# Kernel tuning notes

Hardware: AMD Instinct MI355X
Metric: run time of the kernel (lower is better)

The kernel has to match this reference:

```python
import jax, jax.numpy as jnp
import numpy as np

EPS = 1e-5

def _layernorm(x, g, b):
    mu = jnp.mean(x, axis=-1, keepdims=True)
    var = jnp.mean(jnp.square(x - mu), axis=-1, keepdims=True)
    return (x - mu) * jax.lax.rsqrt(var + EPS) * g + b

def setup_inputs() -> dict:
    key = jax.random.key(0)
    ks = jax.random.split(key, 5)
    T, B, C, E, V = 196, 64, 1024, 512, 32000
    return {
        "feat": jax.random.normal(ks[0], (T, B, C), dtype=jnp.float32),
        "tgt_lang_toks": jax.random.randint(ks[1], (B,), 0, 8),
        "embed_table": jax.random.normal(ks[2], (V, E), dtype=jnp.float32) * 0.02,
        "embed_ln_g": jnp.ones((E,), jnp.float32),
        "embed_ln_b": jnp.zeros((E,), jnp.float32),
        "feat_ln_g": jnp.ones((C,), jnp.float32),
        "feat_ln_b": jnp.zeros((C,), jnp.float32),
        "W1": jax.random.normal(ks[3], (E, E), dtype=jnp.float32) * 0.02,
        "b1": jnp.zeros((E,), jnp.float32),
        "W2": jax.random.normal(ks[4], (C * E, E), dtype=jnp.float32) * 0.02,
        "b2": jnp.zeros((C * E,), jnp.float32),
    }

def reference(feat, tgt_lang_toks, embed_table, embed_ln_g, embed_ln_b,
              feat_ln_g, feat_ln_b, W1, b1, W2, b2):
    # feat: [T, B, C]; tgt_lang_toks: [B]
    T, B, C = feat.shape
    E = W1.shape[0]
    # Per-batch-element dynamic weight generation (same math as the per-unique-token
    # loop: identical tokens produce identical weight matrices).
    emb = embed_table[tgt_lang_toks]                       # [B, E]
    emb = _layernorm(emb, embed_ln_g, embed_ln_b)
    h = jax.nn.relu(emb @ W1.T + b1)                       # [B, E]  (dropout in eval mode)
    w = jax.nn.relu(h @ W2.T + b2)                         # [B, C*E]
    Wmap = w.reshape(B, E, C)                              # per-language mapping matrix
    featn = _layernorm(feat, feat_ln_g, feat_ln_b)         # [T, B, C]
    # out[t,b,e] = sum_c featn[t,b,c] * Wmap[b,e,c]
    out = jnp.einsum('tbc,bec->tbe', featn, Wmap)
    return out
```

## Files before the change

kernel.cpp:

```cpp
#include <hip/hip_runtime.h>
#include <hip/hip_bf16.h>
#include <hip/hip_fp16.h>

typedef _Float16 half8 __attribute__((ext_vector_type(8)));
typedef _Float16 half4v __attribute__((ext_vector_type(4)));
typedef float f32x4 __attribute__((ext_vector_type(4)));

#define T_DIM 196
#define B_DIM 64
#define C_DIM 1024
#define E_DIM 512
#define CE (C_DIM * E_DIM)
#define LN_EPS 1e-5f

#define META_OFF 0
#define H_OFF 4096
#define FEATN_OFF 135168
#define WMAP_OFF 25825280

__global__ void k_prep(const int* __restrict__ toks, int* __restrict__ meta) {
    __shared__ int st[B_DIM];
    int tid = threadIdx.x;
    if (tid < B_DIM) st[tid] = toks[tid];
    __syncthreads();
    if (tid == 0) {
        int ut[B_DIM];
        int inv[B_DIM];
        int ucount = 0;
        for (int b = 0; b < B_DIM; ++b) {
            int t = st[b];
            int slot = -1;
            for (int j = 0; j < ucount; ++j)
                if (ut[j] == t) { slot = j; break; }
            if (slot < 0) { slot = ucount; ut[ucount++] = t; }
            inv[b] = slot;
        }
        meta[0] = ucount;
        for (int b = 0; b < B_DIM; ++b) meta[1 + b] = inv[b];
        for (int j = 0; j < B_DIM; ++j) meta[65 + j] = (j < ucount) ? ut[j] : 0;
    }
}

__global__ __launch_bounds__(256) void k_gen_h(
        const float* __restrict__ embed_table, const float* __restrict__ g,
        const float* __restrict__ bb, const float* __restrict__ W1,
        const float* __restrict__ b1, const int* __restrict__ meta,
        float* __restrict__ h) {
    int u = blockIdx.x;
    int ucount = meta[0];
    int tid = threadIdx.x;
    if (u >= ucount) {
        h[(size_t)u * E_DIM + tid] = 0.0f;
        h[(size_t)u * E_DIM + tid + 256] = 0.0f;
        return;
    }
    int tok = meta[65 + u];
    const float* row = embed_table + (size_t)tok * E_DIM;
    float x0 = row[tid], x1 = row[tid + 256];
    float s = x0 + x1, sq = x0 * x0 + x1 * x1;
    #pragma unroll
    for (int m = 1; m < 64; m <<= 1) { s += __shfl_xor(s, m, 64); sq += __shfl_xor(sq, m, 64); }
    __shared__ float red[4][2];
    int wv = tid >> 6, ln = tid & 63;
    if (ln == 0) { red[wv][0] = s; red[wv][1] = sq; }
    __syncthreads();
    s = red[0][0] + red[1][0] + red[2][0] + red[3][0];
    sq = red[0][1] + red[1][1] + red[2][1] + red[3][1];
    float mu = s * (1.0f / E_DIM);
    float rs = rsqrtf(sq * (1.0f / E_DIM) - mu * mu + LN_EPS);
    __shared__ float lnv[E_DIM];
    lnv[tid] = (x0 - mu) * rs * g[tid] + bb[tid];
    lnv[tid + 256] = (x1 - mu) * rs * g[tid + 256] + bb[tid + 256];
    __syncthreads();
    #pragma unroll
    for (int cc = 0; cc < 2; ++cc) {
        int col = tid + cc * 256;
        const float* wrow = W1 + (size_t)col * E_DIM;
        float acc = b1[col];
        for (int k = 0; k < E_DIM; k += 4) {
            float4 w = *(const float4*)(wrow + k);
            float4 l4 = *(const float4*)(&lnv[k]);
            acc += w.x * l4.x + w.y * l4.y + w.z * l4.z + w.w * l4.w;
        }
        h[(size_t)u * E_DIM + col] = fmaxf(acc, 0.0f);
    }
}

__global__ __launch_bounds__(256) void k_featn(
        const float* __restrict__ feat, const float* __restrict__ g,
        const float* __restrict__ bb, _Float16* __restrict__ featn) {
    int r = blockIdx.x;
    int t = r / B_DIM, b = r % B_DIM;
    const float* x = feat + (size_t)r * C_DIM;
    int tid = threadIdx.x;
    float4 v = *(const float4*)(x + tid * 4);
    float s = v.x + v.y + v.z + v.w;
    float sq = v.x * v.x + v.y * v.y + v.z * v.z + v.w * v.w;
    #pragma unroll
    for (int m = 1; m < 64; m <<= 1) { s += __shfl_xor(s, m, 64); sq += __shfl_xor(sq, m, 64); }
    __shared__ float red[4][2];
    int wv = tid >> 6, ln = tid & 63;
    if (ln == 0) { red[wv][0] = s; red[wv][1] = sq; }
    __syncthreads();
    s = red[0][0] + red[1][0] + red[2][0] + red[3][0];
    sq = red[0][1] + red[1][1] + red[2][1] + red[3][1];
    float mu = s * (1.0f / C_DIM);
    float rs = rsqrtf(sq * (1.0f / C_DIM) - mu * mu + LN_EPS);
    float4 gv = *(const float4*)(g + tid * 4);
    float4 bv = *(const float4*)(bb + tid * 4);
    half4v o;
    o[0] = (_Float16)((v.x - mu) * rs * gv.x + bv.x);
    o[1] = (_Float16)((v.y - mu) * rs * gv.y + bv.y);
    o[2] = (_Float16)((v.z - mu) * rs * gv.z + bv.z);
    o[3] = (_Float16)((v.w - mu) * rs * gv.w + bv.w);
    *(half4v*)(featn + ((size_t)b * T_DIM + t) * C_DIM + tid * 4) = o;
}

__global__ __launch_bounds__(256) void k_wmap(
        const float* __restrict__ W2, const float* __restrict__ b2,
        const float* __restrict__ h, const int* __restrict__ meta,
        _Float16* __restrict__ wmap, int cap) {
    int ucount = meta[0];
    if (ucount > cap) ucount = cap;
    int tid = threadIdx.x;
    int lane = tid & 63;
    int gwave = blockIdx.x * (blockDim.x >> 6) + (tid >> 6);
    int nwaves = gridDim.x * (blockDim.x >> 6);
    int fr = lane & 15, fq = lane >> 4;
    __shared__ _Float16 hseg[16][64][8];
    for (int sg = 0; sg < ucount; sg += 16) {
        __syncthreads();
        {
            int pfr = tid & 15, pks = tid >> 4;
            const float* hp = h + (size_t)(sg + pfr) * E_DIM + pks * 32;
            #pragma unroll
            for (int pq = 0; pq < 4; ++pq) {
                float4 a = *(const float4*)(hp + pq * 8);
                float4 b = *(const float4*)(hp + pq * 8 + 4);
                half8 v;
                v[0] = (_Float16)a.x; v[1] = (_Float16)a.y;
                v[2] = (_Float16)a.z; v[3] = (_Float16)a.w;
                v[4] = (_Float16)b.x; v[5] = (_Float16)b.y;
                v[6] = (_Float16)b.z; v[7] = (_Float16)b.w;
                *(half8*)(&hseg[pks][pq * 16 + pfr][0]) = v;
            }
        }
        __syncthreads();
        int nu = ucount - sg;
        for (long g = gwave; g < (long)(CE / 16); g += nwaves) {
            long i0 = g * 16;
            const float* ap = W2 + (size_t)(i0 + fr) * E_DIM + fq * 8;
            f32x4 acc = {};
            #pragma unroll 4
            for (int ks = 0; ks < 16; ++ks) {
                float4 x0 = *(const float4*)(ap + ks * 32);
                float4 x1 = *(const float4*)(ap + ks * 32 + 4);
                half8 bf = *(const half8*)(&hseg[ks][lane][0]);
                half8 af;
                af[0] = (_Float16)x0.x; af[1] = (_Float16)x0.y;
                af[2] = (_Float16)x0.z; af[3] = (_Float16)x0.w;
                af[4] = (_Float16)x1.x; af[5] = (_Float16)x1.y;
                af[6] = (_Float16)x1.z; af[7] = (_Float16)x1.w;
                acc = __builtin_amdgcn_mfma_f32_16x16x32_f16(af, bf, acc, 0, 0, 0);
            }
            if (fr < nu) {
                float4 bv = *(const float4*)(b2 + i0 + fq * 4);
                half4v o;
                o[0] = (_Float16)fmaxf(acc[0] + bv.x, 0.0f);
                o[1] = (_Float16)fmaxf(acc[1] + bv.y, 0.0f);
                o[2] = (_Float16)fmaxf(acc[2] + bv.z, 0.0f);
                o[3] = (_Float16)fmaxf(acc[3] + bv.w, 0.0f);
                *(half4v*)(wmap + (size_t)(sg + fr) * CE + i0 + fq * 4) = o;
            }
        }
    }
}

__global__ __launch_bounds__(256) void k_einsum(
        const _Float16* __restrict__ featn, const _Float16* __restrict__ wmap,
        const int* __restrict__ meta, float* __restrict__ out, int cap) {
    int b = blockIdx.z;
    int s = meta[1 + b];
    if (s >= cap) s = cap - 1;
    int M0 = blockIdx.y * 128;
    int N0 = blockIdx.x * 128;
    __shared__ _Float16 As[4][128][8];
    __shared__ _Float16 Bs[4][128][8];
    const _Float16* Abase = featn + (size_t)b * T_DIM * C_DIM;
    const _Float16* Bbase = wmap + (size_t)s * CE + (size_t)N0 * C_DIM;
    int tid = threadIdx.x;
    int lane = tid & 63, wv = tid >> 6;
    int wrow = (wv >> 1) * 64, wcol = (wv & 1) * 64;
    int fr = lane & 15, fq = lane >> 4;
    f32x4 acc[4][4] = {};
    for (int kt = 0; kt < C_DIM / 32; ++kt) {
        int k0 = kt * 32;
        #pragma unroll
        for (int hh = 0; hh < 2; ++hh) {
            int id = tid + hh * 256;
            int r = id >> 2, q = id & 3;
            int t = M0 + r;
            uint4 av = make_uint4(0u, 0u, 0u, 0u);
            if (t < T_DIM) av = *(const uint4*)(Abase + (size_t)t * C_DIM + k0 + q * 8);
            *(uint4*)(&As[q][r][0]) = av;
            uint4 bvv = *(const uint4*)(Bbase + (size_t)r * C_DIM + k0 + q * 8);
            *(uint4*)(&Bs[q][r][0]) = bvv;
        }
        __syncthreads();
        half8 af[4], bf[4];
        #pragma unroll
        for (int mi = 0; mi < 4; ++mi) af[mi] = *(const half8*)(&As[fq][wrow + mi * 16 + fr][0]);
        #pragma unroll
        for (int ni = 0; ni < 4; ++ni) bf[ni] = *(const half8*)(&Bs[fq][wcol + ni * 16 + fr][0]);
        #pragma unroll
        for (int mi = 0; mi < 4; ++mi) {
            #pragma unroll
            for (int ni = 0; ni < 4; ++ni) {
                acc[mi][ni] = __builtin_amdgcn_mfma_f32_16x16x32_f16(af[mi], bf[ni], acc[mi][ni], 0, 0, 0);
            }
        }
        __syncthreads();
    }
    #pragma unroll
    for (int mi = 0; mi < 4; ++mi) {
        #pragma unroll
        for (int ni = 0; ni < 4; ++ni) {
            #pragma unroll
            for (int j = 0; j < 4; ++j) {
                int t = M0 + wrow + mi * 16 + fq * 4 + j;
                int e = N0 + wcol + ni * 16 + fr;
                if (t < T_DIM)
                    out[((size_t)t * B_DIM + b) * E_DIM + e] = acc[mi][ni][j];
            }
        }
    }
}

extern "C" void kernel_launch(void* const* d_in, const int* in_sizes, int n_in,
                              void* d_out, int out_size, void* d_ws, size_t ws_size,
                              hipStream_t stream) {
    const float* feat = (const float*)d_in[0];
    const int* toks = (const int*)d_in[1];
    const float* embed_table = (const float*)d_in[2];
    const float* eg = (const float*)d_in[3];
    const float* ebv = (const float*)d_in[4];
    const float* fg = (const float*)d_in[5];
    const float* fb = (const float*)d_in[6];
    const float* W1 = (const float*)d_in[7];
    const float* b1 = (const float*)d_in[8];
    const float* W2 = (const float*)d_in[9];
    const float* b2 = (const float*)d_in[10];
    float* out = (float*)d_out;

    char* ws = (char*)d_ws;
    int* meta = (int*)(ws + META_OFF);
    float* h = (float*)(ws + H_OFF);
    _Float16* featn = (_Float16*)(ws + FEATN_OFF);
    _Float16* wmap = (_Float16*)(ws + WMAP_OFF);

    long cap = 1;
    if (ws_size > (size_t)WMAP_OFF)
        cap = (long)((ws_size - (size_t)WMAP_OFF) / ((size_t)CE * 2));
    if (cap > 64) cap = 64;
    if (cap < 1) cap = 1;

    hipLaunchKernelGGL(k_prep, dim3(1), dim3(64), 0, stream, toks, meta);
    hipLaunchKernelGGL(k_gen_h, dim3(64), dim3(256), 0, stream,
                       embed_table, eg, ebv, W1, b1, meta, h);
    hipLaunchKernelGGL(k_featn, dim3(T_DIM * B_DIM), dim3(256), 0, stream,
                       feat, fg, fb, featn);
    hipLaunchKernelGGL(k_wmap, dim3(2048), dim3(256), 0, stream,
                       W2, b2, h, meta, wmap, (int)cap);
    hipLaunchKernelGGL(k_einsum, dim3(4, 2, 64), dim3(256), 0, stream,
                       featn, wmap, meta, out, (int)cap);
}
```

Before: 347.6 us.

## Stage W2 tiles through swizzled LDS with per-wave double-buffered prefetch

k_wmap now streams each 16-row W2 tile in four 128-column quarters, loading them with fully coalesced float4 row reads into a per-wave double-buffered, XOR-swizzled LDS buffer. The next quarter's loads are issued before the MFMAs on the current quarter, so global latency overlaps compute. The grid is halved to 1024 blocks. This replaces strided per-lane global reads that had poor coalescing, at the cost of 64KB of LDS per block, which limits occupancy, and more register pressure from the prefetch values.

```diff
diff --git a/kernel.cpp b/kernel.cpp
--- a/kernel.cpp
+++ b/kernel.cpp
@@ -124,10 +124,17 @@
     if (ucount > cap) ucount = cap;
     int tid = threadIdx.x;
     int lane = tid & 63;
-    int gwave = blockIdx.x * (blockDim.x >> 6) + (tid >> 6);
-    int nwaves = gridDim.x * (blockDim.x >> 6);
+    int wid = tid >> 6;
     int fr = lane & 15, fq = lane >> 4;
+    int l5 = lane >> 5;
+    int c31 = lane & 31;
+    __shared__ float sbuf[4][2][16][128];
     __shared__ _Float16 hseg[16][64][8];
+
+    long nwaves = (long)gridDim.x * 4;
+    long gw = (long)blockIdx.x * 4 + wid;
+    const long NT = CE / 16;
+
     for (int sg = 0; sg < ucount; sg += 16) {
         __syncthreads();
         {
@@ -147,30 +154,76 @@
         }
         __syncthreads();
         int nu = ucount - sg;
-        for (long g = gwave; g < (long)(CE / 16); g += nwaves) {
-            long i0 = g * 16;
-            const float* ap = W2 + (size_t)(i0 + fr) * E_DIM + fq * 8;
+
+        long ntiles = (gw < NT) ? ((NT - gw + nwaves - 1) / nwaves) : 0;
+        if (ntiles > 0) {
+            long nq = ntiles * 4;
+            {
+                long i0 = gw * 16;
+                #pragma unroll
+                for (int s = 0; s < 8; ++s) {
+                    int row = 2 * s + l5;
+                    float4 rv = *(const float4*)(W2 + (size_t)(i0 + row) * E_DIM + c31 * 4);
+                    *(float4*)(&sbuf[wid][0][row][(c31 ^ (row & 7)) * 4]) = rv;
+                }
+            }
             f32x4 acc = {};
-            #pragma unroll 4
-            for (int ks = 0; ks < 16; ++ks) {
-                float4 x0 = *(const float4*)(ap + ks * 32);
-                float4 x1 = *(const float4*)(ap + ks * 32 + 4);
-                half8 bf = *(const half8*)(&hseg[ks][lane][0]);
-                half8 af;
-                af[0] = (_Float16)x0.x; af[1] = (_Float16)x0.y;
-                af[2] = (_Float16)x0.z; af[3] = (_Float16)x0.w;
-                af[4] = (_Float16)x1.x; af[5] = (_Float16)x1.y;
-                af[6] = (_Float16)x1.z; af[7] = (_Float16)x1.w;
-                acc = __builtin_amdgcn_mfma_f32_16x16x32_f16(af, bf, acc, 0, 0, 0);
-            }
-            if (fr < nu) {
-                float4 bv = *(const float4*)(b2 + i0 + fq * 4);
-                half4v o;
-                o[0] = (_Float16)fmaxf(acc[0] + bv.x, 0.0f);
-                o[1] = (_Float16)fmaxf(acc[1] + bv.y, 0.0f);
-                o[2] = (_Float16)fmaxf(acc[2] + bv.z, 0.0f);
-                o[3] = (_Float16)fmaxf(acc[3] + bv.w, 0.0f);
-                *(half4v*)(wmap + (size_t)(sg + fr) * CE + i0 + fq * 4) = o;
+            for (long qq = 0; qq < nq; ++qq) {
+                int cur = (int)(qq & 1);
+                bool have = (qq + 1 < nq);
+                float4 rr0, rr1, rr2, rr3, rr4, rr5, rr6, rr7;
+                if (have) {
+                    long g2 = gw + ((qq + 1) >> 2) * nwaves;
+                    int qn = (int)((qq + 1) & 3);
+                    const float* base = W2 + (size_t)(g2 * 16) * E_DIM + qn * 128 + c31 * 4;
+                    rr0 = *(const float4*)(base + (size_t)(0  + l5) * E_DIM);
+                    rr1 = *(const float4*)(base + (size_t)(2  + l5) * E_DIM);
+                    rr2 = *(const float4*)(base + (size_t)(4  + l5) * E_DIM);
+                    rr3 = *(const float4*)(base + (size_t)(6  + l5) * E_DIM);
+                    rr4 = *(const float4*)(base + (size_t)(8  + l5) * E_DIM);
+                    rr5 = *(const float4*)(base + (size_t)(10 + l5) * E_DIM);
+                    rr6 = *(const float4*)(base + (size_t)(12 + l5) * E_DIM);
+                    rr7 = *(const float4*)(base + (size_t)(14 + l5) * E_DIM);
+                    __builtin_amdgcn_sched_barrier(0);
+                }
+                int q = (int)(qq & 3);
+                #pragma unroll
+                for (int ks = 0; ks < 4; ++ks) {
+                    int c0 = ks * 8 + fq * 2;
+                    float4 x0 = *(const float4*)(&sbuf[wid][cur][fr][(c0 ^ (fr & 7)) * 4]);
+                    float4 x1 = *(const float4*)(&sbuf[wid][cur][fr][((c0 + 1) ^ (fr & 7)) * 4]);
+                    half8 af;
+                    af[0] = (_Float16)x0.x; af[1] = (_Float16)x0.y;
+                    af[2] = (_Float16)x0.z; af[3] = (_Float16)x0.w;
+                    af[4] = (_Float16)x1.x; af[5] = (_Float16)x1.y;
+                    af[6] = (_Float16)x1.z; af[7] = (_Float16)x1.w;
+                    half8 bf = *(const half8*)(&hseg[q * 4 + ks][lane][0]);
+                    acc = __builtin_amdgcn_mfma_f32_16x16x32_f16(af, bf, acc, 0, 0, 0);
+                }
+                if (q == 3) {
+                    long i0 = (gw + (qq >> 2) * nwaves) * 16;
+                    if (fr < nu) {
+                        float4 bv = *(const float4*)(b2 + i0 + fq * 4);
+                        half4v o;
+                        o[0] = (_Float16)fmaxf(acc[0] + bv.x, 0.0f);
+                        o[1] = (_Float16)fmaxf(acc[1] + bv.y, 0.0f);
+                        o[2] = (_Float16)fmaxf(acc[2] + bv.z, 0.0f);
+                        o[3] = (_Float16)fmaxf(acc[3] + bv.w, 0.0f);
+                        *(half4v*)(wmap + (size_t)(sg + fr) * CE + i0 + fq * 4) = o;
+                    }
+                    acc[0] = 0.0f; acc[1] = 0.0f; acc[2] = 0.0f; acc[3] = 0.0f;
+                }
+                if (have) {
+                    int nb = cur ^ 1;
+                    *(float4*)(&sbuf[wid][nb][0  + l5][(c31 ^ ((0  + l5) & 7)) * 4]) = rr0;
+                    *(float4*)(&sbuf[wid][nb][2  + l5][(c31 ^ ((2  + l5) & 7)) * 4]) = rr1;
+                    *(float4*)(&sbuf[wid][nb][4  + l5][(c31 ^ ((4  + l5) & 7)) * 4]) = rr2;
+                    *(float4*)(&sbuf[wid][nb][6  + l5][(c31 ^ ((6  + l5) & 7)) * 4]) = rr3;
+                    *(float4*)(&sbuf[wid][nb][8  + l5][(c31 ^ ((8  + l5) & 7)) * 4]) = rr4;
+                    *(float4*)(&sbuf[wid][nb][10 + l5][(c31 ^ ((10 + l5) & 7)) * 4]) = rr5;
+                    *(float4*)(&sbuf[wid][nb][12 + l5][(c31 ^ ((12 + l5) & 7)) * 4]) = rr6;
+                    *(float4*)(&sbuf[wid][nb][14 + l5][(c31 ^ ((14 + l5) & 7)) * 4]) = rr7;
+                }
             }
         }
     }
@@ -269,7 +322,7 @@
                        embed_table, eg, ebv, W1, b1, meta, h);
     hipLaunchKernelGGL(k_featn, dim3(T_DIM * B_DIM), dim3(256), 0, stream,
                        feat, fg, fb, featn);
-    hipLaunchKernelGGL(k_wmap, dim3(2048), dim3(256), 0, stream,
+    hipLaunchKernelGGL(k_wmap, dim3(1024), dim3(256), 0, stream,
                        W2, b2, h, meta, wmap, (int)cap);
     hipLaunchKernelGGL(k_einsum, dim3(4, 2, 64), dim3(256), 0, stream,
                        featn, wmap, meta, out, (int)cap);
```

Measured after the change: 332.9 us. 4.2% less time.

## Stage W2 tiles through double-buffered swizzled LDS with split-K wave reduction

Applied to the files above, without the earlier changes.

The W2×h GEMV-like kernel now loads each 16-row W2 tile with coalesced float4 reads into registers, converts it to fp16 and writes it into a double-buffered, XOR-swizzled LDS buffer, prefetching the next tile while computing the current one. The four waves split the K dimension and reduce their partial MFMA results through shared memory. The grid drops from 2048 to 512 blocks. The aim is to replace strided per-lane W2 reads with coalesced streaming and hide HBM latency. In exchange it adds a block-wide barrier per tile and more LDS use, which may lower occupancy.

```diff
diff --git a/kernel.cpp b/kernel.cpp
--- a/kernel.cpp
+++ b/kernel.cpp
@@ -124,10 +124,19 @@
     if (ucount > cap) ucount = cap;
     int tid = threadIdx.x;
     int lane = tid & 63;
-    int gwave = blockIdx.x * (blockDim.x >> 6) + (tid >> 6);
-    int nwaves = gridDim.x * (blockDim.x >> 6);
+    int kw = tid >> 6;
     int fr = lane & 15, fq = lane >> 4;
+    int u8 = tid & 127;
+    int c0 = u8 >> 1;
+
+    __shared__ _Float16 buf[2][16][512];
     __shared__ _Float16 hseg[16][64][8];
+    __shared__ float red[2][4][64][4];
+
+    const long NT = CE / 16;
+    long nb = gridDim.x;
+    long bid = blockIdx.x;
+
     for (int sg = 0; sg < ucount; sg += 16) {
         __syncthreads();
         {
@@ -145,32 +154,89 @@
                 *(half8*)(&hseg[pks][pq * 16 + pfr][0]) = v;
             }
         }
+        int nu = ucount - sg; if (nu > 16) nu = 16;
+
+        {
+            const float* tp = W2 + (size_t)bid * 8192;
+            float4 s0 = *(const float4*)(tp + 0 * 1024 + tid * 4);
+            float4 s1 = *(const float4*)(tp + 1 * 1024 + tid * 4);
+            float4 s2 = *(const float4*)(tp + 2 * 1024 + tid * 4);
+            float4 s3 = *(const float4*)(tp + 3 * 1024 + tid * 4);
+            float4 s4 = *(const float4*)(tp + 4 * 1024 + tid * 4);
+            float4 s5 = *(const float4*)(tp + 5 * 1024 + tid * 4);
+            float4 s6 = *(const float4*)(tp + 6 * 1024 + tid * 4);
+            float4 s7 = *(const float4*)(tp + 7 * 1024 + tid * 4);
+            float4 rr[8] = {s0, s1, s2, s3, s4, s5, s6, s7};
+            #pragma unroll
+            for (int j = 0; j < 8; ++j) {
+                int row = j * 2 + (tid >> 7);
+                int cp = c0 ^ (row & 7);
+                half4v o;
+                o[0] = (_Float16)rr[j].x; o[1] = (_Float16)rr[j].y;
+                o[2] = (_Float16)rr[j].z; o[3] = (_Float16)rr[j].w;
+                *(half4v*)((char*)(&buf[0][0][0]) + row * 1024 + cp * 16 + (u8 & 1) * 8) = o;
+            }
+        }
         __syncthreads();
-        int nu = ucount - sg;
-        for (long g = gwave; g < (long)(CE / 16); g += nwaves) {
-            long i0 = g * 16;
-            const float* ap = W2 + (size_t)(i0 + fr) * E_DIM + fq * 8;
+
+        long ntile = (NT - bid + nb - 1) / nb;
+        for (long n = 0; n < ntile; ++n) {
+            long tt = bid + n * nb;
+            int bb = (int)(n & 1);
+            bool have = (n + 1 < ntile);
+            float4 r0, r1, r2, r3, r4, r5, r6, r7;
+            if (have) {
+                const float* tp = W2 + (size_t)(tt + nb) * 8192;
+                r0 = *(const float4*)(tp + 0 * 1024 + tid * 4);
+                r1 = *(const float4*)(tp + 1 * 1024 + tid * 4);
+                r2 = *(const float4*)(tp + 2 * 1024 + tid * 4);
+                r3 = *(const float4*)(tp + 3 * 1024 + tid * 4);
+                r4 = *(const float4*)(tp + 4 * 1024 + tid * 4);
+                r5 = *(const float4*)(tp + 5 * 1024 + tid * 4);
+                r6 = *(const float4*)(tp + 6 * 1024 + tid * 4);
+                r7 = *(const float4*)(tp + 7 * 1024 + tid * 4);
+                __builtin_amdgcn_sched_barrier(0);
+            }
             f32x4 acc = {};
-            #pragma unroll 4
-            for (int ks = 0; ks < 16; ++ks) {
-                float4 x0 = *(const float4*)(ap + ks * 32);
-                float4 x1 = *(const float4*)(ap + ks * 32 + 4);
-                half8 bf = *(const half8*)(&hseg[ks][lane][0]);
-                half8 af;
-                af[0] = (_Float16)x0.x; af[1] = (_Float16)x0.y;
-                af[2] = (_Float16)x0.z; af[3] = (_Float16)x0.w;
-                af[4] = (_Float16)x1.x; af[5] = (_Float16)x1.y;
-                af[6] = (_Float16)x1.z; af[7] = (_Float16)x1.w;
+            const char* bp = (const char*)(&buf[bb][0][0]);
+            #pragma unroll
+            for (int ks = 0; ks < 4; ++ks) {
+                int cp = (kw * 16 + ks * 4 + fq) ^ (fr & 7);
+                half8 af = *(const half8*)(bp + fr * 1024 + cp * 16);
+                half8 bf = *(const half8*)(&hseg[kw * 4 + ks][lane][0]);
                 acc = __builtin_amdgcn_mfma_f32_16x16x32_f16(af, bf, acc, 0, 0, 0);
             }
-            if (fr < nu) {
-                float4 bv = *(const float4*)(b2 + i0 + fq * 4);
-                half4v o;
-                o[0] = (_Float16)fmaxf(acc[0] + bv.x, 0.0f);
-                o[1] = (_Float16)fmaxf(acc[1] + bv.y, 0.0f);
-                o[2] = (_Float16)fmaxf(acc[2] + bv.z, 0.0f);
-                o[3] = (_Float16)fmaxf(acc[3] + bv.w, 0.0f);
-                *(half4v*)(wmap + (size_t)(sg + fr) * CE + i0 + fq * 4) = o;
+            *(f32x4*)(&red[bb][kw][lane][0]) = acc;
+            if (have) {
+                float4 rr[8] = {r0, r1, r2, r3, r4, r5, r6, r7};
+                char* wp = (char*)(&buf[bb ^ 1][0][0]);
+                #pragma unroll
+                for (int j = 0; j < 8; ++j) {
+                    int row = j * 2 + (tid >> 7);
+                    int cp = c0 ^ (row & 7);
+                    half4v o;
+                    o[0] = (_Float16)rr[j].x; o[1] = (_Float16)rr[j].y;
+                    o[2] = (_Float16)rr[j].z; o[3] = (_Float16)rr[j].w;
+                    *(half4v*)(wp + row * 1024 + cp * 16 + (u8 & 1) * 8) = o;
+                }
+            }
+            __syncthreads();
+            if (kw == 0) {
+                f32x4 s0 = *(const f32x4*)(&red[bb][0][lane][0]);
+                f32x4 s1 = *(const f32x4*)(&red[bb][1][lane][0]);
+                f32x4 s2 = *(const f32x4*)(&red[bb][2][lane][0]);
+                f32x4 s3 = *(const f32x4*)(&red[bb][3][lane][0]);
+                f32x4 s = (s0 + s1) + (s2 + s3);
+                if (fr < nu) {
+                    long i0 = tt * 16;
+                    float4 bv = *(const float4*)(b2 + i0 + fq * 4);
+                    half4v o;
+                    o[0] = (_Float16)fmaxf(s[0] + bv.x, 0.0f);
+                    o[1] = (_Float16)fmaxf(s[1] + bv.y, 0.0f);
+                    o[2] = (_Float16)fmaxf(s[2] + bv.z, 0.0f);
+                    o[3] = (_Float16)fmaxf(s[3] + bv.w, 0.0f);
+                    *(half4v*)(wmap + (size_t)(sg + fr) * CE + i0 + fq * 4) = o;
+                }
             }
         }
     }
@@ -269,7 +335,7 @@
                        embed_table, eg, ebv, W1, b1, meta, h);
     hipLaunchKernelGGL(k_featn, dim3(T_DIM * B_DIM), dim3(256), 0, stream,
                        feat, fg, fb, featn);
-    hipLaunchKernelGGL(k_wmap, dim3(2048), dim3(256), 0, stream,
+    hipLaunchKernelGGL(k_wmap, dim3(512), dim3(256), 0, stream,
                        W2, b2, h, meta, wmap, (int)cap);
     hipLaunchKernelGGL(k_einsum, dim3(4, 2, 64), dim3(256), 0, stream,
                        featn, wmap, meta, out, (int)cap);
```

Measured after the change: 344.9 us. About the same (-0.8%).

## Stream W2 tiles through triple-buffered LDS with async global-to-LDS loads

Applied to the files above, without the earlier changes.

Rewrites the weight-generation kernel so each block processes a contiguous run of 16-row W2 tiles. The tiles are prefetched two ahead into a swizzled triple LDS buffer using direct global-to-LDS loads, with K split across the four waves and reduced through LDS. The grid shrinks from 2048 to 256 blocks. The goal is to keep the memory-bound W2 read streaming with deep prefetch and coalesced contiguous reads. The cost is high LDS use per block, low occupancy, extra barriers per tile, and hand-tuned waitcnt values.

```diff
diff --git a/kernel.cpp b/kernel.cpp
--- a/kernel.cpp
+++ b/kernel.cpp
@@ -17,6 +17,11 @@
 #define H_OFF 4096
 #define FEATN_OFF 135168
 #define WMAP_OFF 25825280
+
+#define WAITV(N) do { asm volatile("s_waitcnt vmcnt(" #N ")" ::: "memory"); \
+                      __builtin_amdgcn_sched_barrier(0); } while (0)
+#define WAITL()  do { asm volatile("s_waitcnt lgkmcnt(0)" ::: "memory"); \
+                      __builtin_amdgcn_sched_barrier(0); } while (0)
 
 __global__ void k_prep(const int* __restrict__ toks, int* __restrict__ meta) {
     __shared__ int st[B_DIM];
@@ -116,6 +121,23 @@
     *(half4v*)(featn + ((size_t)b * T_DIM + t) * C_DIM + tid * 4) = o;
 }
 
+__device__ __forceinline__ void stage_tile(const float* __restrict__ W2,
+                                           float (*buf)[16][512], int bi, long tt,
+                                           int wid, int lane) {
+    const float* g = W2 + (size_t)tt * 8192;
+    #pragma unroll
+    for (int j = 0; j < 8; ++j) {
+        int row = 4 * wid + (j >> 1);
+        int chl = (j & 1) * 64 + lane;
+        int chg = chl ^ ((row & 7) << 1);
+        const float* src = g + (size_t)row * 512 + (size_t)chg * 4;
+        char* dst = (char*)(&buf[bi][0][0]) + row * 2048 + (j & 1) * 1024;
+        __builtin_amdgcn_global_load_lds((const __attribute__((address_space(1))) void*)src,
+                                         (__attribute__((address_space(3))) void*)dst,
+                                         16, 0, 0);
+    }
+}
+
 __global__ __launch_bounds__(256) void k_wmap(
         const float* __restrict__ W2, const float* __restrict__ b2,
         const float* __restrict__ h, const int* __restrict__ meta,
@@ -124,12 +146,19 @@
     if (ucount > cap) ucount = cap;
     int tid = threadIdx.x;
     int lane = tid & 63;
-    int gwave = blockIdx.x * (blockDim.x >> 6) + (tid >> 6);
-    int nwaves = gridDim.x * (blockDim.x >> 6);
+    int wid = tid >> 6;
     int fr = lane & 15, fq = lane >> 4;
+
+    __shared__ float buf[3][16][512];
     __shared__ _Float16 hseg[16][64][8];
+    __shared__ float red[4][64][4];
+
+    const int NB = 128;
+    long tb = (long)blockIdx.x * NB;
+
     for (int sg = 0; sg < ucount; sg += 16) {
-        __syncthreads();
+        stage_tile(W2, buf, 0, tb + 0, wid, lane);
+        stage_tile(W2, buf, 1, tb + 1, wid, lane);
         {
             int pfr = tid & 15, pks = tid >> 4;
             const float* hp = h + (size_t)(sg + pfr) * E_DIM + pks * 32;
@@ -145,34 +174,64 @@
                 *(half8*)(&hseg[pks][pq * 16 + pfr][0]) = v;
             }
         }
+        int nu = ucount - sg; if (nu > 16) nu = 16;
         __syncthreads();
-        int nu = ucount - sg;
-        for (long g = gwave; g < (long)(CE / 16); g += nwaves) {
-            long i0 = g * 16;
-            const float* ap = W2 + (size_t)(i0 + fr) * E_DIM + fq * 8;
+
+        int bi = 0;
+        for (int n = 0; n < NB; ++n) {
+            if (n + 2 < NB) {
+                int bn = bi + 2; if (bn >= 3) bn -= 3;
+                stage_tile(W2, buf, bn, tb + n + 2, wid, lane);
+            }
+            if (n <= NB - 3) {
+                if (wid == 0) { WAITV(18); } else { WAITV(16); }
+            } else if (n == NB - 2) {
+                if (wid == 0) { WAITV(10); } else { WAITV(8); }
+            } else {
+                WAITV(0);
+            }
+            __builtin_amdgcn_s_barrier();
+
             f32x4 acc = {};
-            #pragma unroll 4
-            for (int ks = 0; ks < 16; ++ks) {
-                float4 x0 = *(const float4*)(ap + ks * 32);
-                float4 x1 = *(const float4*)(ap + ks * 32 + 4);
-                half8 bf = *(const half8*)(&hseg[ks][lane][0]);
+            const char* bp = (const char*)(&buf[bi][0][0]);
+            #pragma unroll
+            for (int ks = 0; ks < 4; ++ks) {
+                int c0 = wid * 32 + ks * 8 + fq * 2;
+                int cp = c0 ^ ((fr & 7) << 1);
+                float4 x0 = *(const float4*)(bp + fr * 2048 + cp * 16);
+                float4 x1 = *(const float4*)(bp + fr * 2048 + cp * 16 + 16);
                 half8 af;
                 af[0] = (_Float16)x0.x; af[1] = (_Float16)x0.y;
                 af[2] = (_Float16)x0.z; af[3] = (_Float16)x0.w;
                 af[4] = (_Float16)x1.x; af[5] = (_Float16)x1.y;
                 af[6] = (_Float16)x1.z; af[7] = (_Float16)x1.w;
+                half8 bf = *(const half8*)(&hseg[wid * 4 + ks][lane][0]);
                 acc = __builtin_amdgcn_mfma_f32_16x16x32_f16(af, bf, acc, 0, 0, 0);
             }
-            if (fr < nu) {
-                float4 bv = *(const float4*)(b2 + i0 + fq * 4);
-                half4v o;
-                o[0] = (_Float16)fmaxf(acc[0] + bv.x, 0.0f);
-                o[1] = (_Float16)fmaxf(acc[1] + bv.y, 0.0f);
-                o[2] = (_Float16)fmaxf(acc[2] + bv.z, 0.0f);
-                o[3] = (_Float16)fmaxf(acc[3] + bv.w, 0.0f);
-                *(half4v*)(wmap + (size_t)(sg + fr) * CE + i0 + fq * 4) = o;
-            }
-        }
+            *(f32x4*)(&red[wid][lane][0]) = acc;
+            WAITL();
+            __builtin_amdgcn_s_barrier();
+
+            if (wid == 0) {
+                f32x4 s0 = *(const f32x4*)(&red[0][lane][0]);
+                f32x4 s1 = *(const f32x4*)(&red[1][lane][0]);
+                f32x4 s2 = *(const f32x4*)(&red[2][lane][0]);
+                f32x4 s3 = *(const f32x4*)(&red[3][lane][0]);
+                f32x4 s = (s0 + s1) + (s2 + s3);
+                if (fr < nu) {
+                    long i0 = (tb + n) * 16;
+                    float4 bv = *(const float4*)(b2 + i0 + fq * 4);
+                    half4v o;
+                    o[0] = (_Float16)fmaxf(s[0] + bv.x, 0.0f);
+                    o[1] = (_Float16)fmaxf(s[1] + bv.y, 0.0f);
+                    o[2] = (_Float16)fmaxf(s[2] + bv.z, 0.0f);
+                    o[3] = (_Float16)fmaxf(s[3] + bv.w, 0.0f);
+                    *(half4v*)(wmap + (size_t)(sg + fr) * CE + i0 + fq * 4) = o;
+                }
+            }
+            ++bi; if (bi >= 3) bi = 0;
+        }
+        __syncthreads();
     }
 }
 
@@ -269,7 +328,7 @@
                        embed_table, eg, ebv, W1, b1, meta, h);
     hipLaunchKernelGGL(k_featn, dim3(T_DIM * B_DIM), dim3(256), 0, stream,
                        feat, fg, fb, featn);
-    hipLaunchKernelGGL(k_wmap, dim3(2048), dim3(256), 0, stream,
+    hipLaunchKernelGGL(k_wmap, dim3(256), dim3(256), 0, stream,
                        W2, b2, h, meta, wmap, (int)cap);
     hipLaunchKernelGGL(k_einsum, dim3(4, 2, 64), dim3(256), 0, stream,
                        featn, wmap, meta, out, (int)cap);
```

New measurement: 405.8 us. 16.7% more time.
